# Kernel tuning notes

Hardware: AMD Instinct MI355X
Metric: run time of the kernel (lower is better)

Reference implementation:

```python
import jax, jax.numpy as jnp
import numpy as np

N = 50000        # graph_size / n_nodes
E = 1250000      # n_edges
NFEAT = 128
NHID = 64
NCLASS = 47
NLAYERS = 4
DT = 1.0
ALPHA = 1.0


def setup_inputs() -> dict:
    key = jax.random.key(0)
    ks = jax.random.split(key, 12)
    stdv = 1.0 / np.sqrt(NHID)  # reset_params uses uniform(-1/sqrt(nhid), 1/sqrt(nhid))
    u = lambda k, shp: jax.random.uniform(k, shp, jnp.float32, -stdv, stdv)
    return {
        "x": jax.random.normal(ks[0], (N, NFEAT), jnp.float32),
        "edge_index": jax.random.randint(ks[1], (2, E), 0, N, jnp.int32),
        # Linear weights stored as (in, out); torch computes x @ W.T + b, same math.
        "enc_w": u(ks[2], (NFEAT, NHID)),
        "enc_b": u(ks[3], (NHID,)),
        "conv_w": u(ks[4], (NHID, NHID)),   # GCNConv.lin weight (no bias)
        "conv_b": u(ks[5], (NHID,)),        # GCNConv bias (added after aggregation)
        "res_w": u(ks[6], (NHID, NHID)),
        "res_b": u(ks[7], (NHID,)),
        "dec_w": u(ks[8], (NHID, NCLASS)),
        "dec_b": u(ks[9], (NCLASS,)),
        # original inits epsilons to zeros; small noise makes the gate nontrivial
        "epsilons": 0.01 * jax.random.normal(ks[10], (NLAYERS, NHID), jnp.float32),
    }


def reference(x, edge_index, enc_w, enc_b, conv_w, conv_b, res_w, res_b,
              dec_w, dec_b, epsilons):
    n = x.shape[0]
    loop = jnp.arange(n, dtype=edge_index.dtype)
    row = jnp.concatenate([edge_index[0], loop])  # add self-loops (PyG default)
    col = jnp.concatenate([edge_index[1], loop])
    deg = jax.ops.segment_sum(jnp.ones_like(row, x.dtype), col, num_segments=n)
    dinv = jnp.where(deg > 0, jax.lax.rsqrt(deg), 0.0)
    norm = dinv[row] * dinv[col]  # D^{-1/2} (A+I) D^{-1/2}

    # eval mode: dropout is identity
    X = jax.nn.relu(x @ enc_w + enc_b)
    X0 = X
    for i in range(NLAYERS):
        h = X @ conv_w  # conv.lin(X), shared by conv and residual v1
        conv_out = jax.ops.segment_sum(h[row] * norm[:, None], col,
                                       num_segments=n) + conv_b
        res = -(h @ res_w + res_b)          # res_connection_v1
        coeff = 1.0 + jnp.tanh(epsilons[i])[None, :]  # (1, nhid) broadcast over nodes
        X0 = X0 * coeff + DT * (jax.nn.relu(conv_out + res) - ALPHA * X)
        X = X0
    return X @ dec_w + dec_b
```

## Files before the change

kernel.cpp:

```cpp
#include <hip/hip_runtime.h>
#include <hip/hip_bf16.h>
#include <math.h>

#define NFEAT 128
#define NHID 64
#define NCLASS 47
#define NLAYERS 4
#define CAP 80
#define NBUCK 128
#define BSHIFT 9
#define BSLICE 512
#define BCAP 16384
#define BK_EPB 2048
#define AFW 72
#define XEW 136

typedef __attribute__((ext_vector_type(8))) _Float16 half8;
typedef __attribute__((ext_vector_type(4))) float f32x4;


__global__ __launch_bounds__(256) void k_init(int* __restrict__ gcur,
                                              const float* __restrict__ enc_w,
                                              const float* __restrict__ conv_w,
                                              const float* __restrict__ res_w,
                                              const float* __restrict__ conv_b,
                                              const float* __restrict__ res_b,
                                              const float* __restrict__ eps,
                                              const float* __restrict__ dec_w,
                                              _Float16* __restrict__ Enchb,
                                              _Float16* __restrict__ Whb,
                                              _Float16* __restrict__ W2hb,
                                              _Float16* __restrict__ Dechb,
                                              float* __restrict__ bc,
                                              float* __restrict__ te) {
    int t = blockIdx.x * 256 + threadIdx.x;
    if (t < 1024) {
        int jt = t >> 8, kt = (t >> 6) & 3, l = t & 63;
        int j = jt * 16 + (l & 15);
        int kb = kt * 32 + (l >> 4) * 8;
#pragma unroll
        for (int i = 0; i < 8; ++i)
            Enchb[t * 8 + i] = (_Float16)enc_w[(kb + i) * 64 + j];
        return;
    }
    t -= 1024;
    if (t < 512) {
        int jt = t >> 7, kt = (t >> 6) & 1, l = t & 63;
        int j = jt * 16 + (l & 15);
        int kb = kt * 32 + (l >> 4) * 8;
#pragma unroll
        for (int i = 0; i < 8; ++i)
            Whb[t * 8 + i] = (_Float16)conv_w[(kb + i) * 64 + j];
        return;
    }
    t -= 512;
    if (t < 512) {
        int jt = t >> 7, kt = (t >> 6) & 1, l = t & 63;
        int j = jt * 16 + (l & 15);
        int kb = kt * 32 + (l >> 4) * 8;
#pragma unroll
        for (int i = 0; i < 8; ++i) {
            int k = kb + i;
            float acc = 0.0f;
#pragma unroll 8
            for (int o = 0; o < 64; ++o)
                acc = fmaf(conv_w[k * 64 + o], res_w[o * 64 + j], acc);
            W2hb[t * 8 + i] = (_Float16)acc;
        }
        return;
    }
    t -= 512;
    if (t < 512) {
        int jt = t >> 7, kt = (t >> 6) & 1, l = t & 63;
        int j = jt * 16 + (l & 15);
        int kb = kt * 32 + (l >> 4) * 8;
#pragma unroll
        for (int i = 0; i < 8; ++i) {
            int k = kb + i;
            Dechb[t * 8 + i] = (j < NCLASS) ? (_Float16)dec_w[k * NCLASS + j]
                                            : (_Float16)0.0f;
        }
        return;
    }
    t -= 512;
    if (t < NLAYERS * NHID) {
        te[t] = tanhf(eps[t]);
        if (t < NHID) bc[t] = conv_b[t] - res_b[t];
        if (t < NBUCK) gcur[t] = 0;
    }
}


__global__ __launch_bounds__(256) void k_bucket(const int* __restrict__ row,
                                                const int* __restrict__ col,
                                                int* __restrict__ gcur,
                                                unsigned int* __restrict__ buckets,
                                                int e) {
    __shared__ int lc[BK_EPB];
    __shared__ int lr[BK_EPB];
    __shared__ int cnt[NBUCK], basep[NBUCK], cnt2[NBUCK];
    const int tid = threadIdx.x;
    const int start = blockIdx.x * BK_EPB;
    const int m = min(BK_EPB, e - start);
    for (int i = tid; i < NBUCK; i += 256) { cnt[i] = 0; cnt2[i] = 0; }
    __syncthreads();
    for (int i = tid; i < m; i += 256) {
        int c = col[start + i];
        int r = row[start + i];
        lc[i] = c; lr[i] = r;
        atomicAdd(&cnt[c >> BSHIFT], 1);
    }
    __syncthreads();
    for (int i = tid; i < NBUCK; i += 256)
        if (cnt[i] > 0) basep[i] = atomicAdd(&gcur[i], cnt[i]);
    __syncthreads();
    for (int i = tid; i < m; i += 256) {
        int c = lc[i], r = lr[i];
        int s = c >> BSHIFT;
        int dst = basep[s] + atomicAdd(&cnt2[s], 1);
        if (dst < BCAP)
            buckets[(size_t)s * BCAP + dst] = ((unsigned)r << 16) | (unsigned)c;
    }
}


__global__ __launch_bounds__(256) void k_fill2(const unsigned int* __restrict__ buckets,
                                               const int* __restrict__ gcur,
                                               int* __restrict__ deg,
                                               unsigned short* __restrict__ csr,
                                               int n) {
    __shared__ int cur[BSLICE];
    const int s = blockIdx.x;
    const int tid = threadIdx.x;
    for (int i = tid; i < BSLICE; i += 256) cur[i] = 0;
    __syncthreads();
    const int cnt = min(gcur[s], BCAP);
    const unsigned int* bp = buckets + (size_t)s * BCAP;
    for (int i = tid; i < cnt; i += 256) {
        unsigned int v = bp[i];
        int c = (int)(v & 0xffffu);
        int r = (int)(v >> 16);
        int pos = atomicAdd(&cur[c & (BSLICE - 1)], 1);
        if (pos < CAP) csr[(size_t)c * CAP + pos] = (unsigned short)r;
    }
    __syncthreads();
    const int base = s * BSLICE;
    const int nb = min(BSLICE, n - base);
    for (int i = tid; i < nb; i += 256) deg[base + i] = cur[i];
}


__global__ void k_dinv(const int* __restrict__ deg, float* __restrict__ dinv,
                       float* __restrict__ rsq, unsigned short* __restrict__ csr,
                       _Float16* __restrict__ Y0, _Float16* __restrict__ Y1, int n) {
    int i = blockIdx.x * blockDim.x + threadIdx.x;
    if (i < n) {
        int d = deg[i];
        if (d > CAP) d = CAP;
        float d1 = (float)(deg[i] + 1);
        dinv[i] = rsqrtf(d1);
        rsq[i] = sqrtf(d1);
        int end = (d + 7) & ~7;
        if (end > CAP) end = CAP;
        for (int s = d; s < end; ++s)
            csr[(size_t)i * CAP + s] = (unsigned short)n;
    }
    if (i < NHID) {
        Y0[(size_t)n * NHID + i] = (_Float16)0.0f;
        Y1[(size_t)n * NHID + i] = (_Float16)0.0f;
    }
}


__global__ __launch_bounds__(256) void k_encoder(const float* __restrict__ x,
                                                 const half8* __restrict__ Enchb,
                                                 const float* __restrict__ b,
                                                 const float* __restrict__ dinv,
                                                 _Float16* __restrict__ Y, int n) {
    __shared__ _Float16 Xe[16][XEW];
    const int wid = threadIdx.x >> 6;
    const int lane = threadIdx.x & 63;
    const int base = blockIdx.x * 16 + wid * 4;

    {
        int nl = wid * 4 + ((threadIdx.x >> 4) & 3);
        int seg = threadIdx.x & 15;
        int node = blockIdx.x * 16 + nl;
        float4 u = make_float4(0.f, 0.f, 0.f, 0.f), v = u;
        if (node < n) {
            const float4* xp = reinterpret_cast<const float4*>(x + (size_t)node * NFEAT + seg * 8);
            u = xp[0]; v = xp[1];
        }
        half8 h;
        h[0] = (_Float16)u.x; h[1] = (_Float16)u.y; h[2] = (_Float16)u.z; h[3] = (_Float16)u.w;
        h[4] = (_Float16)v.x; h[5] = (_Float16)v.y; h[6] = (_Float16)v.z; h[7] = (_Float16)v.w;
        *reinterpret_cast<half8*>(&Xe[nl][seg * 8]) = h;
    }

    const int ar = (wid * 4 + (lane & 15)) & 15;
    const int aq = (lane >> 4) * 8;
    half8 a0 = *reinterpret_cast<const half8*>(&Xe[ar][0 * 32 + aq]);
    half8 a1 = *reinterpret_cast<const half8*>(&Xe[ar][1 * 32 + aq]);
    half8 a2 = *reinterpret_cast<const half8*>(&Xe[ar][2 * 32 + aq]);
    half8 a3 = *reinterpret_cast<const half8*>(&Xe[ar][3 * 32 + aq]);
    const f32x4 zero = {0.f, 0.f, 0.f, 0.f};

    float dvv[4];
#pragma unroll
    for (int i = 0; i < 4; ++i) dvv[i] = (base + i < n) ? dinv[base + i] : 0.f;

#pragma unroll
    for (int jt = 0; jt < 4; ++jt) {
        f32x4 dacc = __builtin_amdgcn_mfma_f32_16x16x32_f16(a0, Enchb[(jt * 4 + 0) * 64 + lane], zero, 0, 0, 0);
        dacc = __builtin_amdgcn_mfma_f32_16x16x32_f16(a1, Enchb[(jt * 4 + 1) * 64 + lane], dacc, 0, 0, 0);
        dacc = __builtin_amdgcn_mfma_f32_16x16x32_f16(a2, Enchb[(jt * 4 + 2) * 64 + lane], dacc, 0, 0, 0);
        dacc = __builtin_amdgcn_mfma_f32_16x16x32_f16(a3, Enchb[(jt * 4 + 3) * 64 + lane], dacc, 0, 0, 0);
        if (lane < 16) {
            int j = jt * 16 + lane;
            float bj = b[j];
#pragma unroll
            for (int i = 0; i < 4; ++i) {
                int node = base + i;
                if (node < n) {
                    float v = fmaxf(dacc[i] + bj, 0.0f);
                    Y[(size_t)node * NHID + j] = (_Float16)(v * dvv[i]);
                }
            }
        }
    }
}


__global__ __launch_bounds__(256, 4) void k_layer(
    const half8* __restrict__ Y8c, _Float16* __restrict__ Ynext,
    const int* __restrict__ deg, const unsigned short* __restrict__ csr,
    const float* __restrict__ dinv, const float* __restrict__ rsq,
    const half8* __restrict__ Whb, const half8* __restrict__ W2hb,
    const half8* __restrict__ Dechb,
    const float* __restrict__ bc, const float* __restrict__ te,
    const float* __restrict__ dec_b, float* __restrict__ out, int n, int last) {
    __shared__ _Float16 Af[16][AFW];
    __shared__ _Float16 Xf[16][AFW];
    const int wid = threadIdx.x >> 6;
    const int lane = threadIdx.x & 63;
    const int g = lane >> 4;
    const int l = lane & 15;
    const int c = l & 7;
    const unsigned sh = (l & 8) << 1;
    const int base = blockIdx.x * 16 + wid * 4;
    const int mynode = base + g;
    const bool gact = mynode < n;
    const int gn = gact ? mynode : 0;
    const int rown = gact ? mynode : n;
    const float dcg = dinv[gn];
    const float rcg = rsq[gn];
    int d = gact ? deg[gn] : 0;
    if (d > CAP) d = CAP;
    const int nit = (d + 7) >> 3;

    float acc[8] = {0.f, 0.f, 0.f, 0.f, 0.f, 0.f, 0.f, 0.f};
    const uint4* cp = reinterpret_cast<const uint4*>(csr + (size_t)gn * CAP);

    uint4 rt = cp[0];
    int a0 = (int)((rt.x >> sh) & 0xffffu);
    int a1 = (int)((rt.y >> sh) & 0xffffu);
    int a2 = (int)((rt.z >> sh) & 0xffffu);
    int a3 = (int)((rt.w >> sh) & 0xffffu);
    half8 A0 = Y8c[(size_t)(a0 * 8 + c)];
    half8 A1 = Y8c[(size_t)(a1 * 8 + c)];
    half8 A2 = Y8c[(size_t)(a2 * 8 + c)];
    half8 A3 = Y8c[(size_t)(a3 * 8 + c)];
    rt = cp[1];
    int b0 = (int)((rt.x >> sh) & 0xffffu);
    int b1 = (int)((rt.y >> sh) & 0xffffu);
    int b2 = (int)((rt.z >> sh) & 0xffffu);
    int b3 = (int)((rt.w >> sh) & 0xffffu);
    half8 B0 = Y8c[(size_t)(b0 * 8 + c)];
    half8 B1 = Y8c[(size_t)(b1 * 8 + c)];
    half8 B2 = Y8c[(size_t)(b2 * 8 + c)];
    half8 B3 = Y8c[(size_t)(b3 * 8 + c)];
    uint4 rc2 = cp[2];
    int it = 0;
    for (; it + 2 < nit; ++it) {
        int c0 = (int)((rc2.x >> sh) & 0xffffu);
        int c1 = (int)((rc2.y >> sh) & 0xffffu);
        int c2 = (int)((rc2.z >> sh) & 0xffffu);
        int c3 = (int)((rc2.w >> sh) & 0xffffu);
        half8 C0 = Y8c[(size_t)(c0 * 8 + c)];
        half8 C1 = Y8c[(size_t)(c1 * 8 + c)];
        half8 C2 = Y8c[(size_t)(c2 * 8 + c)];
        half8 C3 = Y8c[(size_t)(c3 * 8 + c)];
        rc2 = cp[it + 3];
#pragma unroll
        for (int i = 0; i < 8; ++i)
            acc[i] += ((float)A0[i] + (float)A1[i]) + ((float)A2[i] + (float)A3[i]);
        A0 = B0; A1 = B1; A2 = B2; A3 = B3;
        B0 = C0; B1 = C1; B2 = C2; B3 = C3;
    }
    if (it < nit) {
#pragma unroll
        for (int i = 0; i < 8; ++i)
            acc[i] += ((float)A0[i] + (float)A1[i]) + ((float)A2[i] + (float)A3[i]);
    }
    if (it + 1 < nit) {
#pragma unroll
        for (int i = 0; i < 8; ++i)
            acc[i] += ((float)B0[i] + (float)B1[i]) + ((float)B2[i] + (float)B3[i]);
    }
#pragma unroll
    for (int i = 0; i < 8; ++i) acc[i] += __shfl_xor(acc[i], 8);

    if (l < 8) {
        half8 yc = Y8c[(size_t)(rown * 8 + c)];
        half8 hg, hx;
#pragma unroll
        for (int i = 0; i < 8; ++i) {
            float ycf = (float)yc[i];
            hg[i] = (_Float16)((acc[i] + ycf) * dcg);
            hx[i] = (_Float16)(ycf * rcg);
        }
        *reinterpret_cast<half8*>(&Af[wid * 4 + g][c * 8]) = hg;
        *reinterpret_cast<half8*>(&Xf[wid * 4 + g][c * 8]) = hx;
    }

    float dv[4];
#pragma unroll
    for (int i = 0; i < 4; ++i) dv[i] = __shfl(dcg, i * 16);

    const int ar = (wid * 4 + (lane & 15)) & 15;
    const int aq = (lane >> 4) * 8;
    half8 aG0 = *reinterpret_cast<const half8*>(&Af[ar][aq]);
    half8 aG1 = *reinterpret_cast<const half8*>(&Af[ar][32 + aq]);
    half8 aX0 = *reinterpret_cast<const half8*>(&Xf[ar][aq]);
    half8 aX1 = *reinterpret_cast<const half8*>(&Xf[ar][32 + aq]);
    const f32x4 zero = {0.f, 0.f, 0.f, 0.f};

#pragma unroll
    for (int jt = 0; jt < 4; ++jt) {
        half8 bG0 = Whb[(jt * 2 + 0) * 64 + lane];
        half8 bG1 = Whb[(jt * 2 + 1) * 64 + lane];
        half8 bX0 = W2hb[(jt * 2 + 0) * 64 + lane];
        half8 bX1 = W2hb[(jt * 2 + 1) * 64 + lane];
        f32x4 dG = __builtin_amdgcn_mfma_f32_16x16x32_f16(aG0, bG0, zero, 0, 0, 0);
        dG = __builtin_amdgcn_mfma_f32_16x16x32_f16(aG1, bG1, dG, 0, 0, 0);
        f32x4 dX = __builtin_amdgcn_mfma_f32_16x16x32_f16(aX0, bX0, zero, 0, 0, 0);
        dX = __builtin_amdgcn_mfma_f32_16x16x32_f16(aX1, bX1, dX, 0, 0, 0);
        if (lane < 16) {
            int j = jt * 16 + lane;
            float tej = te[j], bcj = bc[j];
#pragma unroll
            for (int i = 0; i < 4; ++i) {
                int node = base + i;
                float xf = (float)Xf[wid * 4 + i][j];
                float xn = xf * tej + fmaxf(dG[i] + bcj - dX[i], 0.0f);
                if (!last) {
                    if (node < n)
                        Ynext[(size_t)node * NHID + j] = (_Float16)(xn * dv[i]);
                } else {
                    Af[wid * 4 + i][j] = (_Float16)xn;
                }
            }
        }
    }

    if (last) {
        half8 aD0 = *reinterpret_cast<const half8*>(&Af[ar][aq]);
        half8 aD1 = *reinterpret_cast<const half8*>(&Af[ar][32 + aq]);
#pragma unroll
        for (int jt = 0; jt < 4; ++jt) {
            half8 bD0 = Dechb[(jt * 2 + 0) * 64 + lane];
            half8 bD1 = Dechb[(jt * 2 + 1) * 64 + lane];
            f32x4 dd = __builtin_amdgcn_mfma_f32_16x16x32_f16(aD0, bD0, zero, 0, 0, 0);
            dd = __builtin_amdgcn_mfma_f32_16x16x32_f16(aD1, bD1, dd, 0, 0, 0);
            if (lane < 16) {
                int j = jt * 16 + lane;
                if (j < NCLASS) {
                    float db = dec_b[j];
#pragma unroll
                    for (int i = 0; i < 4; ++i) {
                        int node = base + i;
                        if (node < n) out[(size_t)node * NCLASS + j] = dd[i] + db;
                    }
                }
            }
        }
    }
}

extern "C" void kernel_launch(void* const* d_in, const int* in_sizes, int n_in,
                              void* d_out, int out_size, void* d_ws, size_t ws_size,
                              hipStream_t stream) {
    const float* x      = (const float*)d_in[0];
    const int*   edges  = (const int*)d_in[1];
    const float* enc_w  = (const float*)d_in[2];
    const float* enc_b  = (const float*)d_in[3];
    const float* conv_w = (const float*)d_in[4];
    const float* conv_b = (const float*)d_in[5];
    const float* res_w  = (const float*)d_in[6];
    const float* res_b  = (const float*)d_in[7];
    const float* dec_w  = (const float*)d_in[8];
    const float* dec_b  = (const float*)d_in[9];
    const float* eps    = (const float*)d_in[10];
    float* out = (float*)d_out;

    const int n = in_sizes[0] / NFEAT;
    const int e = in_sizes[1] / 2;
    const int* row = edges;
    const int* col = edges + e;

    char* p = (char*)d_ws;
    unsigned short* csr = (unsigned short*)p;
    p += ((size_t)n * CAP * 2 + 64 + 15) & ~(size_t)15;
    unsigned int* buckets = (unsigned int*)p;  p += (size_t)NBUCK * BCAP * 4;
    _Float16* Y0 = (_Float16*)p;  p += (((size_t)(n + 1) * NHID * 2 + 15) & ~(size_t)15);
    _Float16* Y1 = (_Float16*)p;  p += (((size_t)(n + 1) * NHID * 2 + 15) & ~(size_t)15);
    int*   deg  = (int*)p;    p += (size_t)n * 4;
    float* dinv = (float*)p;  p += (size_t)n * 4;
    float* rsq  = (float*)p;  p += (size_t)n * 4;
    int*   gcur = (int*)p;    p += ((NBUCK + 15) & ~15) * 4;
    float* bc   = (float*)p;  p += NHID * 4;
    float* te   = (float*)p;  p += NLAYERS * NHID * 4;
    _Float16* Enchb = (_Float16*)p;  p += 8192 * 2;
    _Float16* Whb   = (_Float16*)p;  p += 4096 * 2;
    _Float16* W2hb  = (_Float16*)p;  p += 4096 * 2;
    _Float16* Dechb = (_Float16*)p;  p += 4096 * 2;
    if ((size_t)(p - (char*)d_ws) > ws_size) return;

    k_init<<<11, 256, 0, stream>>>(gcur, enc_w, conv_w, res_w, conv_b, res_b,
                                   eps, dec_w, Enchb, Whb, W2hb, Dechb, bc, te);
    const int bblocks = (e + BK_EPB - 1) / BK_EPB;
    k_bucket<<<bblocks, 256, 0, stream>>>(row, col, gcur, buckets, e);
    k_fill2<<<NBUCK, 256, 0, stream>>>(buckets, gcur, deg, csr, n);
    k_dinv<<<(n + 255) / 256, 256, 0, stream>>>(deg, dinv, rsq, csr, Y0, Y1, n);

    const int tblocks = (n + 15) / 16;
    k_encoder<<<tblocks, 256, 0, stream>>>(x, (const half8*)Enchb, enc_b, dinv, Y0, n);

    for (int l = 0; l < NLAYERS; ++l) {
        _Float16* ycur = (l & 1) ? Y1 : Y0;
        _Float16* ynxt = (l & 1) ? Y0 : Y1;
        k_layer<<<tblocks, 256, 0, stream>>>((const half8*)ycur, ynxt, deg, csr,
                                             dinv, rsq, (const half8*)Whb,
                                             (const half8*)W2hb, (const half8*)Dechb,
                                             bc, te + l * NHID, dec_b, out, n,
                                             (l == NLAYERS - 1) ? 1 : 0);
    }
}
```

Before: 222.9 us.

## Split node feature buffer into two 32-wide planes and gather per plane

The fp16 node feature array is stored as two feature-half planes of 32 columns each instead of one 64-wide row per node. The aggregation loop then runs twice, once per plane, with each 16-lane group covering 4 neighbours of 64 bytes at a time instead of 2 neighbours of 128 bytes. This is meant to shrink the gather working set per pass so it fits better in cache. In exchange, the CSR index rows are read twice and there is an extra shuffle reduction step.

```diff
diff --git a/kernel.cpp b/kernel.cpp
--- a/kernel.cpp
+++ b/kernel.cpp
@@ -165,9 +165,12 @@
         for (int s = d; s < end; ++s)
             csr[(size_t)i * CAP + s] = (unsigned short)n;
     }
-    if (i < NHID) {
-        Y0[(size_t)n * NHID + i] = (_Float16)0.0f;
-        Y1[(size_t)n * NHID + i] = (_Float16)0.0f;
+    if (i < 32) {
+        size_t PSh = (size_t)(n + 1) * 32;
+        Y0[(size_t)n * 32 + i] = (_Float16)0.0f;
+        Y0[PSh + (size_t)n * 32 + i] = (_Float16)0.0f;
+        Y1[(size_t)n * 32 + i] = (_Float16)0.0f;
+        Y1[PSh + (size_t)n * 32 + i] = (_Float16)0.0f;
     }
 }
 
@@ -181,6 +184,7 @@
     const int wid = threadIdx.x >> 6;
     const int lane = threadIdx.x & 63;
     const int base = blockIdx.x * 16 + wid * 4;
+    const size_t PSh = (size_t)(n + 1) * 32;
 
     {
         int nl = wid * 4 + ((threadIdx.x >> 4) & 3);
@@ -223,7 +227,8 @@
                 int node = base + i;
                 if (node < n) {
                     float v = fmaxf(dacc[i] + bj, 0.0f);
-                    Y[(size_t)node * NHID + j] = (_Float16)(v * dvv[i]);
+                    Y[(size_t)(j >> 5) * PSh + (size_t)node * 32 + (j & 31)] =
+                        (_Float16)(v * dvv[i]);
                 }
             }
         }
@@ -245,8 +250,9 @@
     const int lane = threadIdx.x & 63;
     const int g = lane >> 4;
     const int l = lane & 15;
-    const int c = l & 7;
-    const unsigned sh = (l & 8) << 1;
+    const int c = l & 3;
+    const int s = l >> 2;
+    const unsigned sh2 = (unsigned)((s & 1) << 4);
     const int base = blockIdx.x * 16 + wid * 4;
     const int mynode = base + g;
     const bool gact = mynode < n;
@@ -257,70 +263,73 @@
     int d = gact ? deg[gn] : 0;
     if (d > CAP) d = CAP;
     const int nit = (d + 7) >> 3;
-
-    float acc[8] = {0.f, 0.f, 0.f, 0.f, 0.f, 0.f, 0.f, 0.f};
-    const uint4* cp = reinterpret_cast<const uint4*>(csr + (size_t)gn * CAP);
-
-    uint4 rt = cp[0];
-    int a0 = (int)((rt.x >> sh) & 0xffffu);
-    int a1 = (int)((rt.y >> sh) & 0xffffu);
-    int a2 = (int)((rt.z >> sh) & 0xffffu);
-    int a3 = (int)((rt.w >> sh) & 0xffffu);
-    half8 A0 = Y8c[(size_t)(a0 * 8 + c)];
-    half8 A1 = Y8c[(size_t)(a1 * 8 + c)];
-    half8 A2 = Y8c[(size_t)(a2 * 8 + c)];
-    half8 A3 = Y8c[(size_t)(a3 * 8 + c)];
-    rt = cp[1];
-    int b0 = (int)((rt.x >> sh) & 0xffffu);
-    int b1 = (int)((rt.y >> sh) & 0xffffu);
-    int b2 = (int)((rt.z >> sh) & 0xffffu);
-    int b3 = (int)((rt.w >> sh) & 0xffffu);
-    half8 B0 = Y8c[(size_t)(b0 * 8 + c)];
-    half8 B1 = Y8c[(size_t)(b1 * 8 + c)];
-    half8 B2 = Y8c[(size_t)(b2 * 8 + c)];
-    half8 B3 = Y8c[(size_t)(b3 * 8 + c)];
-    uint4 rc2 = cp[2];
-    int it = 0;
-    for (; it + 2 < nit; ++it) {
-        int c0 = (int)((rc2.x >> sh) & 0xffffu);
-        int c1 = (int)((rc2.y >> sh) & 0xffffu);
-        int c2 = (int)((rc2.z >> sh) & 0xffffu);
-        int c3 = (int)((rc2.w >> sh) & 0xffffu);
-        half8 C0 = Y8c[(size_t)(c0 * 8 + c)];
-        half8 C1 = Y8c[(size_t)(c1 * 8 + c)];
-        half8 C2 = Y8c[(size_t)(c2 * 8 + c)];
-        half8 C3 = Y8c[(size_t)(c3 * 8 + c)];
-        rc2 = cp[it + 3];
-#pragma unroll
-        for (int i = 0; i < 8; ++i)
-            acc[i] += ((float)A0[i] + (float)A1[i]) + ((float)A2[i] + (float)A3[i]);
-        A0 = B0; A1 = B1; A2 = B2; A3 = B3;
-        B0 = C0; B1 = C1; B2 = C2; B3 = C3;
-    }
-    if (it < nit) {
-#pragma unroll
-        for (int i = 0; i < 8; ++i)
-            acc[i] += ((float)A0[i] + (float)A1[i]) + ((float)A2[i] + (float)A3[i]);
-    }
-    if (it + 1 < nit) {
-#pragma unroll
-        for (int i = 0; i < 8; ++i)
-            acc[i] += ((float)B0[i] + (float)B1[i]) + ((float)B2[i] + (float)B3[i]);
-    }
-#pragma unroll
-    for (int i = 0; i < 8; ++i) acc[i] += __shfl_xor(acc[i], 8);
-
-    if (l < 8) {
-        half8 yc = Y8c[(size_t)(rown * 8 + c)];
-        half8 hg, hx;
+    const size_t PS8 = (size_t)(n + 1) * 4;
+    const size_t PSh = (size_t)(n + 1) * 32;
+
+    const uint4* cpu4 = reinterpret_cast<const uint4*>(csr + (size_t)gn * CAP);
+
+#pragma unroll
+    for (int p = 0; p < 2; ++p) {
+        const half8* Yp = Y8c + p * PS8;
+        float acc[8] = {0.f, 0.f, 0.f, 0.f, 0.f, 0.f, 0.f, 0.f};
+
+        uint4 rA = cpu4[0];
+        unsigned wa0 = (s >> 1) ? rA.y : rA.x;
+        unsigned wa1 = (s >> 1) ? rA.w : rA.z;
+        int ea0 = (int)((wa0 >> sh2) & 0xffffu);
+        int ea1 = (int)((wa1 >> sh2) & 0xffffu);
+        half8 A0 = Yp[(size_t)ea0 * 4 + c];
+        half8 A1 = Yp[(size_t)ea1 * 4 + c];
+        uint4 rB = cpu4[1];
+        unsigned wb0 = (s >> 1) ? rB.y : rB.x;
+        unsigned wb1 = (s >> 1) ? rB.w : rB.z;
+        int eb0 = (int)((wb0 >> sh2) & 0xffffu);
+        int eb1 = (int)((wb1 >> sh2) & 0xffffu);
+        half8 B0 = Yp[(size_t)eb0 * 4 + c];
+        half8 B1 = Yp[(size_t)eb1 * 4 + c];
+        uint4 rC = cpu4[2];
+        int it = 0;
+        for (; it + 2 < nit; ++it) {
+            unsigned wc0 = (s >> 1) ? rC.y : rC.x;
+            unsigned wc1 = (s >> 1) ? rC.w : rC.z;
+            int ec0 = (int)((wc0 >> sh2) & 0xffffu);
+            int ec1 = (int)((wc1 >> sh2) & 0xffffu);
+            half8 C0 = Yp[(size_t)ec0 * 4 + c];
+            half8 C1 = Yp[(size_t)ec1 * 4 + c];
+            rC = cpu4[it + 3];
+#pragma unroll
+            for (int i = 0; i < 8; ++i)
+                acc[i] += (float)A0[i] + (float)A1[i];
+            A0 = B0; A1 = B1;
+            B0 = C0; B1 = C1;
+        }
+        if (it < nit) {
+#pragma unroll
+            for (int i = 0; i < 8; ++i)
+                acc[i] += (float)A0[i] + (float)A1[i];
+        }
+        if (it + 1 < nit) {
+#pragma unroll
+            for (int i = 0; i < 8; ++i)
+                acc[i] += (float)B0[i] + (float)B1[i];
+        }
 #pragma unroll
         for (int i = 0; i < 8; ++i) {
-            float ycf = (float)yc[i];
-            hg[i] = (_Float16)((acc[i] + ycf) * dcg);
-            hx[i] = (_Float16)(ycf * rcg);
-        }
-        *reinterpret_cast<half8*>(&Af[wid * 4 + g][c * 8]) = hg;
-        *reinterpret_cast<half8*>(&Xf[wid * 4 + g][c * 8]) = hx;
+            acc[i] += __shfl_xor(acc[i], 4);
+            acc[i] += __shfl_xor(acc[i], 8);
+        }
+        if (s == 0) {
+            half8 yc = Yp[(size_t)rown * 4 + c];
+            half8 hg, hx;
+#pragma unroll
+            for (int i = 0; i < 8; ++i) {
+                float ycf = (float)yc[i];
+                hg[i] = (_Float16)((acc[i] + ycf) * dcg);
+                hx[i] = (_Float16)(ycf * rcg);
+            }
+            *reinterpret_cast<half8*>(&Af[wid * 4 + g][p * 32 + c * 8]) = hg;
+            *reinterpret_cast<half8*>(&Xf[wid * 4 + g][p * 32 + c * 8]) = hx;
+        }
     }
 
     float dv[4];
@@ -355,7 +364,8 @@
                 float xn = xf * tej + fmaxf(dG[i] + bcj - dX[i], 0.0f);
                 if (!last) {
                     if (node < n)
-                        Ynext[(size_t)node * NHID + j] = (_Float16)(xn * dv[i]);
+                        Ynext[(size_t)(j >> 5) * PSh + (size_t)node * 32 + (j & 31)] =
+                            (_Float16)(xn * dv[i]);
                 } else {
                     Af[wid * 4 + i][j] = (_Float16)xn;
                 }
@@ -412,8 +422,8 @@
     unsigned short* csr = (unsigned short*)p;
     p += ((size_t)n * CAP * 2 + 64 + 15) & ~(size_t)15;
     unsigned int* buckets = (unsigned int*)p;  p += (size_t)NBUCK * BCAP * 4;
-    _Float16* Y0 = (_Float16*)p;  p += (((size_t)(n + 1) * NHID * 2 + 15) & ~(size_t)15);
-    _Float16* Y1 = (_Float16*)p;  p += (((size_t)(n + 1) * NHID * 2 + 15) & ~(size_t)15);
+    _Float16* Y0 = (_Float16*)p;  p += (((size_t)(n + 1) * NHID * 2 + 127) & ~(size_t)127);
+    _Float16* Y1 = (_Float16*)p;  p += (((size_t)(n + 1) * NHID * 2 + 127) & ~(size_t)127);
     int*   deg  = (int*)p;    p += (size_t)n * 4;
     float* dinv = (float*)p;  p += (size_t)n * 4;
     float* rsq  = (float*)p;  p += (size_t)n * 4;
```

Result: no change. 224.8 us (+0.9%).
